# Performance work log

Measured on AMD Instinct MI355X. Metric: run time of the kernel, lower is better.

Reference implementation:

```python
import jax, jax.numpy as jnp
import numpy as np

EN_HID = 1024
DE_HID = 1024
BATCH = 64
SRC_LEN = 2048


def setup_inputs() -> dict:
    key = jax.random.key(0)
    ks = jax.random.split(key, 7)
    s_en = 1.0 / np.sqrt(EN_HID)
    s_de = 1.0 / np.sqrt(DE_HID)
    return {
        "hidden": jax.random.normal(ks[0], (1, BATCH, DE_HID), jnp.float32),
        "en_output": jax.random.normal(ks[1], (BATCH, SRC_LEN, EN_HID), jnp.float32),
        "w_en_w": jax.random.uniform(ks[2], (DE_HID, EN_HID), jnp.float32, -s_en, s_en),
        "w_en_b": jax.random.uniform(ks[3], (DE_HID,), jnp.float32, -s_en, s_en),
        "w_de_w": jax.random.uniform(ks[4], (DE_HID, DE_HID), jnp.float32, -s_de, s_de),
        "w_de_b": jax.random.uniform(ks[5], (DE_HID,), jnp.float32, -s_de, s_de),
        "v_w": jax.random.uniform(ks[6], (1, DE_HID), jnp.float32, -s_de, s_de),
    }


def reference(hidden, en_output, w_en_w, w_en_b, w_de_w, w_de_b, v_w):
    # hidden: (1, B, Dd) -> (B, 1, Dd); broadcast over src_len instead of repeat
    h = jnp.transpose(hidden, (1, 0, 2))  # (B, 1, Dd)
    proj_en = jnp.einsum('bse,de->bsd', en_output, w_en_w) + w_en_b  # (B, S, Dd)
    proj_de = jnp.einsum('bqh,dh->bqd', h, w_de_w) + w_de_b          # (B, 1, Dd)
    energy = jnp.tanh(proj_en + proj_de)                              # (B, S, Dd)
    scores = jnp.einsum('bsd,od->bs', energy, v_w)                   # (B, S)
    attention = jax.nn.softmax(scores, axis=1)                        # (B, S)
    weighted = jnp.einsum('bs,bse->be', attention, en_output)[:, None, :]  # (B, 1, E)
    return weighted, attention
```

## Files before the change

### kernel.cpp

```cpp
#include <hip/hip_runtime.h>
#include <stdint.h>

typedef __attribute__((ext_vector_type(4))) float  f32x4;
typedef __attribute__((ext_vector_type(8))) short  bf16x8;
typedef __attribute__((ext_vector_type(4))) short  s16x4;

#define BATCH   64
#define SRC_LEN 2048
#define HID     1024
#define M_TOT   (BATCH*SRC_LEN)

#define BM 256
#define BN 256
#define BK 64

__device__ __forceinline__ short f2bf(float f) {
  unsigned u = __builtin_bit_cast(unsigned, f);
  u += 0x7fffu + ((u >> 16) & 1u);
  return (short)(u >> 16);
}
__device__ __forceinline__ float bf2f(short s) {
  unsigned u = ((unsigned)(unsigned short)s) << 16;
  return __builtin_bit_cast(float, u);
}

__global__ void k_convert_w(const float* __restrict__ w, short* __restrict__ wb) {
  int i = (blockIdx.x * 256 + threadIdx.x) * 8;
  f32x4 a = *(const f32x4*)(w + i);
  f32x4 b = *(const f32x4*)(w + i + 4);
  bf16x8 o;
  o[0]=f2bf(a[0]); o[1]=f2bf(a[1]); o[2]=f2bf(a[2]); o[3]=f2bf(a[3]);
  o[4]=f2bf(b[0]); o[5]=f2bf(b[1]); o[6]=f2bf(b[2]); o[7]=f2bf(b[3]);
  *(bf16x8*)(wb + i) = o;
}

__global__ void k_convert_en(const float* __restrict__ in, short* __restrict__ out) {
  size_t stride = (size_t)gridDim.x * 256 * 8;
  size_t base = ((size_t)blockIdx.x * 256 + threadIdx.x) * 8;
  size_t total = (size_t)M_TOT * HID;
  for (; base < total; base += stride) {
    f32x4 a = *(const f32x4*)(in + base);
    f32x4 b = *(const f32x4*)(in + base + 4);
    bf16x8 o;
    o[0]=f2bf(a[0]); o[1]=f2bf(a[1]); o[2]=f2bf(a[2]); o[3]=f2bf(a[3]);
    o[4]=f2bf(b[0]); o[5]=f2bf(b[1]); o[6]=f2bf(b[2]); o[7]=f2bf(b[3]);
    *(bf16x8*)(out + base) = o;
  }
}

__global__ void k_bias(const float* __restrict__ hidden, const float* __restrict__ w_de_w,
                       const float* __restrict__ w_en_b, const float* __restrict__ w_de_b,
                       float* __restrict__ bias_all) {
  __shared__ float hid[HID];
  int b  = blockIdx.x >> 2;
  int dc = blockIdx.x & 3;
  for (int i = threadIdx.x; i < HID; i += 256) hid[i] = hidden[b*HID + i];
  __syncthreads();
  int d = dc*256 + threadIdx.x;
  const f32x4* wrow = (const f32x4*)(w_de_w + (size_t)d*HID);
  float acc = 0.f;
  #pragma unroll 8
  for (int q = 0; q < HID/4; ++q) {
    f32x4 w4 = wrow[q];
    f32x4 h4 = *(const f32x4*)&hid[q*4];
    acc += w4[0]*h4[0] + w4[1]*h4[1] + w4[2]*h4[2] + w4[3]*h4[3];
  }
  bias_all[b*HID + d] = acc + w_en_b[d] + w_de_b[d];
}

__global__ void __launch_bounds__(512, 1) k_gemm_score_fast(
    const short* __restrict__ Abf,
    const short* __restrict__ Bw,
    const float* __restrict__ bias_all,
    const float* __restrict__ v_w,
    float* __restrict__ scores)
{
  __shared__ short As[2][BM][BK];
  __shared__ short Bs[2][BN][BK];

  int raw  = blockIdx.x;
  int xcd  = raw & 7;
  int idx  = raw >> 3;
  int mblk = xcd * 64 + (idx >> 2);
  int nblk = idx & 3;
  int m0 = mblk * BM, n0 = nblk * BN;

  int tid  = threadIdx.x;
  int lane = tid & 63;
  int wid  = tid >> 6;
  int wm = wid >> 2, wn = wid & 3;
  int fr  = lane & 15;
  int fko = (lane >> 4) * 8;
  int rsw = (fr & 7) << 3;

  f32x4 acc[8][4] = {};

  int cA0 = tid,        cA1 = tid + 1024;
  int cA2 = tid + 512,  cA3 = tid + 1536;
  int gb  = ((tid >> 8) << 9) + (tid & 255);
  int cB0 = gb,         cB1 = gb + 1024;
  int cB2 = gb + 256,   cB3 = gb + 1280;

  #define SOFF(c, rb) ((size_t)((rb) + ((c) >> 3)) * HID + (size_t)((((c) & 7) ^ (((c) >> 3) & 7)) * 8))
  const size_t sA0 = SOFF(cA0, m0), sA1 = SOFF(cA1, m0), sA2 = SOFF(cA2, m0), sA3 = SOFF(cA3, m0);
  const size_t sB0 = SOFF(cB0, n0), sB1 = SOFF(cB1, n0), sB2 = SOFF(cB2, n0), sB3 = SOFF(cB3, n0);
  #undef SOFF

  #define GLD(SRCP, LDSBASE, DOFF) __builtin_amdgcn_global_load_lds( \
      (const __attribute__((address_space(1))) void*)(SRCP), \
      (__attribute__((address_space(3))) void*)((char*)(LDSBASE) + (DOFF)), 16, 0, 0)

  #define STG_A01(OTH, KT) do{ GLD(Abf + sA0 + (KT)*64, &As[OTH][0][0], cA0*16); \
                               GLD(Abf + sA1 + (KT)*64, &As[OTH][0][0], cA1*16); }while(0)
  #define STG_A23(OTH, KT) do{ GLD(Abf + sA2 + (KT)*64, &As[OTH][0][0], cA2*16); \
                               GLD(Abf + sA3 + (KT)*64, &As[OTH][0][0], cA3*16); }while(0)
  #define STG_B01(OTH, KT) do{ GLD(Bw  + sB0 + (KT)*64, &Bs[OTH][0][0], cB0*16); \
                               GLD(Bw  + sB1 + (KT)*64, &Bs[OTH][0][0], cB1*16); }while(0)
  #define STG_B23(OTH, KT) do{ GLD(Bw  + sB2 + (KT)*64, &Bs[OTH][0][0], cB2*16); \
                               GLD(Bw  + sB3 + (KT)*64, &Bs[OTH][0][0], cB3*16); }while(0)

  bf16x8 aF[8], bF[4];
  #define LDA(BUF, MQ) { _Pragma("unroll") for (int mi = 0; mi < 4; ++mi) \
      _Pragma("unroll") for (int kk = 0; kk < 2; ++kk) \
        aF[mi*2+kk] = *(const bf16x8*)&As[BUF][wm*128 + (MQ)*64 + mi*16 + fr][(kk*32 + fko) ^ rsw]; }
  #define LDB(BUF, NQ) { _Pragma("unroll") for (int ni = 0; ni < 2; ++ni) \
      _Pragma("unroll") for (int kk = 0; kk < 2; ++kk) \
        bF[ni*2+kk] = *(const bf16x8*)&Bs[BUF][wn*64 + (NQ)*32 + ni*16 + fr][(kk*32 + fko) ^ rsw]; }
  #define MMQ(MQ, NQ) { _Pragma("unroll") for (int mi = 0; mi < 4; ++mi) \
      _Pragma("unroll") for (int ni = 0; ni < 2; ++ni) \
      _Pragma("unroll") for (int kk = 0; kk < 2; ++kk) \
        acc[(MQ)*4+mi][(NQ)*2+ni] = __builtin_amdgcn_mfma_f32_16x16x32_bf16( \
            aF[mi*2+kk], bF[ni*2+kk], acc[(MQ)*4+mi][(NQ)*2+ni], 0, 0, 0); }

  #define BARR   __builtin_amdgcn_s_barrier()
  #define VMC(N) asm volatile("s_waitcnt vmcnt(" #N ")" ::: "memory")
  #define PR1    __builtin_amdgcn_s_setprio(1)
  #define PR0    __builtin_amdgcn_s_setprio(0)

  STG_A01(0, 0); STG_B01(0, 0); STG_B23(0, 0); STG_A23(0, 0);
  VMC(4); BARR;

  #pragma unroll 1
  for (int kt = 0; kt < 15; ++kt) {
    int buf = kt & 1, oth = buf ^ 1;
    LDA(buf, 0); LDB(buf, 0); STG_A01(oth, kt + 1);
    BARR; PR1; MMQ(0, 0); PR0; VMC(4); BARR;
    LDB(buf, 1); STG_B01(oth, kt + 1);
    BARR; PR1; MMQ(0, 1); PR0; VMC(4); BARR;
    LDA(buf, 1); STG_B23(oth, kt + 1);
    BARR; PR1; MMQ(1, 1); PR0; BARR;
    LDB(buf, 0); STG_A23(oth, kt + 1);
    BARR; PR1; MMQ(1, 0); PR0; VMC(4); BARR;
  }
  LDA(1, 0); LDB(1, 0); BARR; PR1; MMQ(0, 0); PR0; VMC(2); BARR;
  LDB(1, 1);            BARR; PR1; MMQ(0, 1); PR0; VMC(0); BARR;
  LDA(1, 1);            BARR; PR1; MMQ(1, 1); PR0; BARR;
  LDB(1, 0);            BARR; PR1; MMQ(1, 0); PR0;

  #undef LDA
  #undef LDB
  #undef MMQ
  #undef STG_A01
  #undef STG_A23
  #undef STG_B01
  #undef STG_B23
  #undef GLD

  int b = m0 >> 11;
  float vv[4], bb[4];
  #pragma unroll
  for (int nf = 0; nf < 4; ++nf) {
    int col = n0 + wn*64 + nf*16 + fr;
    vv[nf] = v_w[col];
    bb[nf] = bias_all[b*HID + col];
  }
  #pragma unroll
  for (int mf = 0; mf < 8; ++mf) {
    #pragma unroll
    for (int j = 0; j < 4; ++j) {
      float p = 0.f;
      #pragma unroll
      for (int nf = 0; nf < 4; ++nf)
        p += tanhf(acc[mf][nf][j] + bb[nf]) * vv[nf];
      p += __shfl_xor(p, 1);
      p += __shfl_xor(p, 2);
      p += __shfl_xor(p, 4);
      p += __shfl_xor(p, 8);
      if (fr == 0) {
        int row = wm*128 + mf*16 + ((lane >> 4) << 2) + j;
        atomicAdd(&scores[m0 + row], p);
      }
    }
  }
}

__global__ void __launch_bounds__(256) k_gemm_score_conv(
    const float* __restrict__ A, const short* __restrict__ Bw,
    const float* __restrict__ bias_all, const float* __restrict__ v_w,
    float* __restrict__ scores)
{
  __shared__ short Asl[128][64];
  __shared__ short Bsl[128][64];
  int raw  = blockIdx.x;
  int xcd  = raw & 7;
  int idx  = raw >> 3;
  int mblk = xcd * (M_TOT/128/8) + (idx >> 3);
  int nblk = idx & 7;
  int m0 = mblk * 128, n0 = nblk * 128;
  int tid  = threadIdx.x;
  int lane = tid & 63;
  int wid  = tid >> 6;
  int wr = wid >> 1, wc = wid & 1;
  int fr  = lane & 15;
  int fko = (lane >> 4) * 8;
  f32x4 acc[4][4] = {};
  int ar = tid >> 1;
  int ac = (tid & 1) * 32;
  const float* aBase = A + (size_t)(m0 + ar) * HID + ac;
  f32x4 aReg[8];
  #pragma unroll
  for (int i = 0; i < 8; ++i) aReg[i] = *(const f32x4*)(aBase + i*4);
  for (int kt = 0; kt < 16; ++kt) {
    __syncthreads();
    #pragma unroll
    for (int g = 0; g < 4; ++g) {
      bf16x8 w;
      w[0]=f2bf(aReg[2*g][0]);   w[1]=f2bf(aReg[2*g][1]);
      w[2]=f2bf(aReg[2*g][2]);   w[3]=f2bf(aReg[2*g][3]);
      w[4]=f2bf(aReg[2*g+1][0]); w[5]=f2bf(aReg[2*g+1][1]);
      w[6]=f2bf(aReg[2*g+1][2]); w[7]=f2bf(aReg[2*g+1][3]);
      *(bf16x8*)&Asl[ar][ac + g*8] = w;
    }
    #pragma unroll
    for (int j = 0; j < 4; ++j) {
      int c = j*256 + tid;
      const short* src = Bw + (size_t)(n0 + (c >> 3)) * HID + kt*64 + (c & 7)*8;
      __builtin_amdgcn_global_load_lds(
          (const __attribute__((address_space(1))) void*)src,
          (__attribute__((address_space(3))) void*)((char*)&Bsl[0][0] + c*16),
          16, 0, 0);
    }
    __syncthreads();
    if (kt + 1 < 16) {
      const float* nxt = aBase + (kt+1)*64;
      #pragma unroll
      for (int i = 0; i < 8; ++i) aReg[i] = *(const f32x4*)(nxt + i*4);
    }
    #pragma unroll
    for (int kk = 0; kk < 2; ++kk) {
      bf16x8 aF[4], bF[4];
      #pragma unroll
      for (int mi = 0; mi < 4; ++mi)
        aF[mi] = *(const bf16x8*)&Asl[wr*64 + mi*16 + fr][kk*32 + fko];
      #pragma unroll
      for (int ni = 0; ni < 4; ++ni)
        bF[ni] = *(const bf16x8*)&Bsl[wc*64 + ni*16 + fr][kk*32 + fko];
      #pragma unroll
      for (int mi = 0; mi < 4; ++mi)
        #pragma unroll
        for (int ni = 0; ni < 4; ++ni)
          acc[mi][ni] = __builtin_amdgcn_mfma_f32_16x16x32_bf16(aF[mi], bF[ni], acc[mi][ni], 0, 0, 0);
    }
  }
  int b = m0 >> 11;
  float vv[4], bb[4];
  #pragma unroll
  for (int ni = 0; ni < 4; ++ni) {
    int col = n0 + wc*64 + ni*16 + fr;
    vv[ni] = v_w[col];
    bb[ni] = bias_all[b*HID + col];
  }
  #pragma unroll
  for (int mi = 0; mi < 4; ++mi) {
    #pragma unroll
    for (int j = 0; j < 4; ++j) {
      float p = 0.f;
      #pragma unroll
      for (int ni = 0; ni < 4; ++ni)
        p += tanhf(acc[mi][ni][j] + bb[ni]) * vv[ni];
      p += __shfl_xor(p, 1);
      p += __shfl_xor(p, 2);
      p += __shfl_xor(p, 4);
      p += __shfl_xor(p, 8);
      if (fr == 0) {
        int row = wr*64 + mi*16 + ((lane >> 4) << 2) + j;
        atomicAdd(&scores[m0 + row], p);
      }
    }
  }
}

__global__ void k_softmax(float* __restrict__ attn) {
  int b = blockIdx.x;
  float* row = attn + (size_t)b * SRC_LEN;
  int tid = threadIdx.x, lane = tid & 63, wid = tid >> 6;
  __shared__ float red[4];
  float v[8];
  #pragma unroll
  for (int i = 0; i < 8; ++i) v[i] = row[tid + i*256];
  float mx = v[0];
  #pragma unroll
  for (int i = 1; i < 8; ++i) mx = fmaxf(mx, v[i]);
  #pragma unroll
  for (int o = 32; o; o >>= 1) mx = fmaxf(mx, __shfl_xor(mx, o));
  if (lane == 0) red[wid] = mx;
  __syncthreads();
  mx = fmaxf(fmaxf(red[0], red[1]), fmaxf(red[2], red[3]));
  float s = 0.f;
  #pragma unroll
  for (int i = 0; i < 8; ++i) { v[i] = __expf(v[i] - mx); s += v[i]; }
  #pragma unroll
  for (int o = 32; o; o >>= 1) s += __shfl_xor(s, o);
  __syncthreads();
  if (lane == 0) red[wid] = s;
  __syncthreads();
  s = red[0] + red[1] + red[2] + red[3];
  float inv = 1.f / s;
  #pragma unroll
  for (int i = 0; i < 8; ++i) row[tid + i*256] = v[i] * inv;
}

__global__ void k_weighted_bf(const short* __restrict__ en_bf, const float* __restrict__ attn,
                              float* __restrict__ outw) {
  int b  = blockIdx.x >> 4;
  int sc = blockIdx.x & 15;
  __shared__ float aw[128];
  int tid = threadIdx.x;
  if (tid < 128) aw[tid] = attn[b*SRC_LEN + sc*128 + tid];
  __syncthreads();
  const short* base = en_bf + ((size_t)b*SRC_LEN + sc*128) * HID + tid*4;
  float a0=0.f, a1=0.f, a2=0.f, a3=0.f;
  #pragma unroll 8
  for (int s = 0; s < 128; ++s) {
    s16x4 x = *(const s16x4*)(base + (size_t)s*HID);
    float w = aw[s];
    a0 += w*bf2f(x[0]); a1 += w*bf2f(x[1]); a2 += w*bf2f(x[2]); a3 += w*bf2f(x[3]);
  }
  float* o = outw + b*HID + tid*4;
  atomicAdd(o+0, a0); atomicAdd(o+1, a1);
  atomicAdd(o+2, a2); atomicAdd(o+3, a3);
}

__global__ void k_weighted(const float* __restrict__ en, const float* __restrict__ attn,
                           float* __restrict__ outw) {
  int b  = blockIdx.x >> 4;
  int sc = blockIdx.x & 15;
  __shared__ float aw[128];
  int tid = threadIdx.x;
  if (tid < 128) aw[tid] = attn[b*SRC_LEN + sc*128 + tid];
  __syncthreads();
  const float* base = en + ((size_t)b*SRC_LEN + sc*128) * HID + tid*4;
  f32x4 acc = {0.f, 0.f, 0.f, 0.f};
  #pragma unroll 8
  for (int s = 0; s < 128; ++s) {
    f32x4 x = *(const f32x4*)(base + (size_t)s*HID);
    float w = aw[s];
    acc[0] += w*x[0]; acc[1] += w*x[1]; acc[2] += w*x[2]; acc[3] += w*x[3];
  }
  float* o = outw + b*HID + tid*4;
  atomicAdd(o+0, acc[0]); atomicAdd(o+1, acc[1]);
  atomicAdd(o+2, acc[2]); atomicAdd(o+3, acc[3]);
}

extern "C" void kernel_launch(void* const* d_in, const int* in_sizes, int n_in,
                              void* d_out, int out_size, void* d_ws, size_t ws_size,
                              hipStream_t stream) {
  const float* hidden = (const float*)d_in[0];
  const float* en     = (const float*)d_in[1];
  const float* w_en_w = (const float*)d_in[2];
  const float* w_en_b = (const float*)d_in[3];
  const float* w_de_w = (const float*)d_in[4];
  const float* w_de_b = (const float*)d_in[5];
  const float* v_w    = (const float*)d_in[6];

  float* outw = (float*)d_out;
  float* attn = outw + BATCH*HID;

  const size_t en_elems = (size_t)M_TOT * HID;
  const size_t need_fast = en_elems*sizeof(short) + (size_t)HID*HID*sizeof(short)
                         + (size_t)BATCH*HID*sizeof(float);

  hipMemsetAsync(d_out, 0, (size_t)out_size * sizeof(float), stream);

  if (ws_size >= need_fast) {
    short* en_bf    = (short*)d_ws;
    short* w_bf     = en_bf + en_elems;
    float* bias_all = (float*)(w_bf + (size_t)HID*HID);

    k_convert_en<<<dim3(2048), dim3(256), 0, stream>>>(en, en_bf);
    k_convert_w<<<dim3(HID*HID/(256*8)), dim3(256), 0, stream>>>(w_en_w, w_bf);
    k_bias<<<dim3(BATCH*4), dim3(256), 0, stream>>>(hidden, w_de_w, w_en_b, w_de_b, bias_all);
    k_gemm_score_fast<<<dim3((M_TOT/BM)*(HID/BN)), dim3(512), 0, stream>>>(en_bf, w_bf, bias_all, v_w, attn);
    k_softmax<<<dim3(BATCH), dim3(256), 0, stream>>>(attn);
    k_weighted_bf<<<dim3(BATCH*16), dim3(256), 0, stream>>>(en_bf, attn, outw);
  } else {
    short* w_bf     = (short*)d_ws;
    float* bias_all = (float*)((char*)d_ws + (size_t)HID*HID*sizeof(short));
    k_convert_w<<<dim3(HID*HID/(256*8)), dim3(256), 0, stream>>>(w_en_w, w_bf);
    k_bias<<<dim3(BATCH*4), dim3(256), 0, stream>>>(hidden, w_de_w, w_en_b, w_de_b, bias_all);
    k_gemm_score_conv<<<dim3((M_TOT/128)*(HID/128)), dim3(256), 0, stream>>>(en, w_bf, bias_all, v_w, attn);
    k_softmax<<<dim3(BATCH), dim3(256), 0, stream>>>(attn);
    k_weighted<<<dim3(BATCH*16), dim3(256), 0, stream>>>(en, attn, outw);
  }
}
```

Measured before the change: 608.8 us.

## Fuse fp32-to-bf16 conversion of encoder outputs into the score GEMM

Removes the separate conversion kernel for en_output. The GEMM now loads fp32 A tiles into registers, converts them to bf16 and writes them into LDS, and one N-block per tile also writes the bf16 copy to global memory for the later weighted-sum kernel. The B tiles still use direct global-to-LDS loads. The main loop is rescheduled around register-staged A loads, and the aim is to save a full read and write pass over the large activation tensor. In exchange, the GEMM reads twice as many A bytes (fp32), is read by four N-blocks, and carries extra conversion ALU work and register pressure.

Result: slower. 646.5 us (+6.2%).

```diff
diff --git a/kernel.cpp b/kernel.cpp
--- a/kernel.cpp
+++ b/kernel.cpp
@@ -23,29 +23,18 @@
   unsigned u = ((unsigned)(unsigned short)s) << 16;
   return __builtin_bit_cast(float, u);
 }
+__device__ __forceinline__ bf16x8 cvt8(f32x4 lo, f32x4 hi) {
+  bf16x8 o;
+  o[0]=f2bf(lo[0]); o[1]=f2bf(lo[1]); o[2]=f2bf(lo[2]); o[3]=f2bf(lo[3]);
+  o[4]=f2bf(hi[0]); o[5]=f2bf(hi[1]); o[6]=f2bf(hi[2]); o[7]=f2bf(hi[3]);
+  return o;
+}
 
 __global__ void k_convert_w(const float* __restrict__ w, short* __restrict__ wb) {
   int i = (blockIdx.x * 256 + threadIdx.x) * 8;
   f32x4 a = *(const f32x4*)(w + i);
   f32x4 b = *(const f32x4*)(w + i + 4);
-  bf16x8 o;
-  o[0]=f2bf(a[0]); o[1]=f2bf(a[1]); o[2]=f2bf(a[2]); o[3]=f2bf(a[3]);
-  o[4]=f2bf(b[0]); o[5]=f2bf(b[1]); o[6]=f2bf(b[2]); o[7]=f2bf(b[3]);
-  *(bf16x8*)(wb + i) = o;
-}
-
-__global__ void k_convert_en(const float* __restrict__ in, short* __restrict__ out) {
-  size_t stride = (size_t)gridDim.x * 256 * 8;
-  size_t base = ((size_t)blockIdx.x * 256 + threadIdx.x) * 8;
-  size_t total = (size_t)M_TOT * HID;
-  for (; base < total; base += stride) {
-    f32x4 a = *(const f32x4*)(in + base);
-    f32x4 b = *(const f32x4*)(in + base + 4);
-    bf16x8 o;
-    o[0]=f2bf(a[0]); o[1]=f2bf(a[1]); o[2]=f2bf(a[2]); o[3]=f2bf(a[3]);
-    o[4]=f2bf(b[0]); o[5]=f2bf(b[1]); o[6]=f2bf(b[2]); o[7]=f2bf(b[3]);
-    *(bf16x8*)(out + base) = o;
-  }
+  *(bf16x8*)(wb + i) = cvt8(a, b);
 }
 
 __global__ void k_bias(const float* __restrict__ hidden, const float* __restrict__ w_de_w,
@@ -68,12 +57,13 @@
   bias_all[b*HID + d] = acc + w_en_b[d] + w_de_b[d];
 }
 
-__global__ void __launch_bounds__(512, 1) k_gemm_score_fast(
-    const short* __restrict__ Abf,
+__global__ void __launch_bounds__(512, 1) k_gemm_score_fused(
+    const float* __restrict__ Af,
     const short* __restrict__ Bw,
     const float* __restrict__ bias_all,
     const float* __restrict__ v_w,
-    float* __restrict__ scores)
+    float* __restrict__ scores,
+    short* __restrict__ en_bf)
 {
   __shared__ short As[2][BM][BK];
   __shared__ short Bs[2][BN][BK];
@@ -95,29 +85,18 @@
 
   f32x4 acc[8][4] = {};
 
-  int cA0 = tid,        cA1 = tid + 1024;
-  int cA2 = tid + 512,  cA3 = tid + 1536;
-  int gb  = ((tid >> 8) << 9) + (tid & 255);
-  int cB0 = gb,         cB1 = gb + 1024;
-  int cB2 = gb + 256,   cB3 = gb + 1280;
-
-  #define SOFF(c, rb) ((size_t)((rb) + ((c) >> 3)) * HID + (size_t)((((c) & 7) ^ (((c) >> 3) & 7)) * 8))
-  const size_t sA0 = SOFF(cA0, m0), sA1 = SOFF(cA1, m0), sA2 = SOFF(cA2, m0), sA3 = SOFF(cA3, m0);
-  const size_t sB0 = SOFF(cB0, n0), sB1 = SOFF(cB1, n0), sB2 = SOFF(cB2, n0), sB3 = SOFF(cB3, n0);
-  #undef SOFF
-
-  #define GLD(SRCP, LDSBASE, DOFF) __builtin_amdgcn_global_load_lds( \
+  int r  = tid >> 3;
+  int sl = tid & 7;
+  int xr = sl ^ (r & 7);
+  size_t offBase = (size_t)(m0 + r) * HID + (size_t)sl * 8;
+  int    wBase   = r * BK + xr * 8;
+  int gbRow = r + ((tid >> 8) << 5);
+  size_t sBase = (size_t)(n0 + gbRow) * HID + (size_t)xr * 8;
+  int gb = ((tid >> 8) << 9) + (tid & 255);
+
+  #define GLD(SRCP, LDSP) __builtin_amdgcn_global_load_lds( \
       (const __attribute__((address_space(1))) void*)(SRCP), \
-      (__attribute__((address_space(3))) void*)((char*)(LDSBASE) + (DOFF)), 16, 0, 0)
-
-  #define STG_A01(OTH, KT) do{ GLD(Abf + sA0 + (KT)*64, &As[OTH][0][0], cA0*16); \
-                               GLD(Abf + sA1 + (KT)*64, &As[OTH][0][0], cA1*16); }while(0)
-  #define STG_A23(OTH, KT) do{ GLD(Abf + sA2 + (KT)*64, &As[OTH][0][0], cA2*16); \
-                               GLD(Abf + sA3 + (KT)*64, &As[OTH][0][0], cA3*16); }while(0)
-  #define STG_B01(OTH, KT) do{ GLD(Bw  + sB0 + (KT)*64, &Bs[OTH][0][0], cB0*16); \
-                               GLD(Bw  + sB1 + (KT)*64, &Bs[OTH][0][0], cB1*16); }while(0)
-  #define STG_B23(OTH, KT) do{ GLD(Bw  + sB2 + (KT)*64, &Bs[OTH][0][0], cB2*16); \
-                               GLD(Bw  + sB3 + (KT)*64, &Bs[OTH][0][0], cB3*16); }while(0)
+      (__attribute__((address_space(3))) void*)(LDSP), 16, 0, 0)
 
   bf16x8 aF[8], bF[4];
   #define LDA(BUF, MQ) { _Pragma("unroll") for (int mi = 0; mi < 4; ++mi) \
@@ -133,37 +112,97 @@
             aF[mi*2+kk], bF[ni*2+kk], acc[(MQ)*4+mi][(NQ)*2+ni], 0, 0, 0); }
 
   #define BARR   __builtin_amdgcn_s_barrier()
+  #define LG0    asm volatile("s_waitcnt lgkmcnt(0)" ::: "memory")
   #define VMC(N) asm volatile("s_waitcnt vmcnt(" #N ")" ::: "memory")
   #define PR1    __builtin_amdgcn_s_setprio(1)
   #define PR0    __builtin_amdgcn_s_setprio(0)
 
-  STG_A01(0, 0); STG_B01(0, 0); STG_B23(0, 0); STG_A23(0, 0);
-  VMC(4); BARR;
+  {
+    short* ldsA = (short*)&As[0][0][0] + wBase;
+    char*  ldsB = (char*)&Bs[0][0][0] + gb*16;
+    f32x4 a0 = *(const f32x4*)(Af + offBase);
+    f32x4 a1 = *(const f32x4*)(Af + offBase + 4);
+    f32x4 a2 = *(const f32x4*)(Af + offBase + 128*HID);
+    f32x4 a3 = *(const f32x4*)(Af + offBase + 128*HID + 4);
+    GLD(Bw + sBase,            ldsB + 0);
+    GLD(Bw + sBase + 128*HID,  ldsB + 16384);
+    bf16x8 av0 = cvt8(a0, a1), av1 = cvt8(a2, a3);
+    *(bf16x8*)(ldsA)        = av0;
+    *(bf16x8*)(ldsA + 8192) = av1;
+    if (nblk == 0) *(bf16x8*)(en_bf + offBase) = av0;
+    if (nblk == 1) *(bf16x8*)(en_bf + offBase + 128*HID) = av1;
+    f32x4 b0 = *(const f32x4*)(Af + offBase + 64*HID);
+    f32x4 b1 = *(const f32x4*)(Af + offBase + 64*HID + 4);
+    f32x4 b2 = *(const f32x4*)(Af + offBase + 192*HID);
+    f32x4 b3 = *(const f32x4*)(Af + offBase + 192*HID + 4);
+    GLD(Bw + sBase + 32*HID,   ldsB + 4096);
+    GLD(Bw + sBase + 160*HID,  ldsB + 20480);
+    bf16x8 av2 = cvt8(b0, b1), av3 = cvt8(b2, b3);
+    *(bf16x8*)(ldsA + 4096)  = av2;
+    *(bf16x8*)(ldsA + 12288) = av3;
+    if (nblk == 2) *(bf16x8*)(en_bf + offBase + 64*HID) = av2;
+    if (nblk == 3) *(bf16x8*)(en_bf + offBase + 192*HID) = av3;
+    LG0; BARR;
+  }
 
   #pragma unroll 1
   for (int kt = 0; kt < 15; ++kt) {
-    int buf = kt & 1, oth = buf ^ 1;
-    LDA(buf, 0); LDB(buf, 0); STG_A01(oth, kt + 1);
-    BARR; PR1; MMQ(0, 0); PR0; VMC(4); BARR;
-    LDB(buf, 1); STG_B01(oth, kt + 1);
-    BARR; PR1; MMQ(0, 1); PR0; VMC(4); BARR;
-    LDA(buf, 1); STG_B23(oth, kt + 1);
-    BARR; PR1; MMQ(1, 1); PR0; BARR;
-    LDB(buf, 0); STG_A23(oth, kt + 1);
-    BARR; PR1; MMQ(1, 0); PR0; VMC(4); BARR;
-  }
-  LDA(1, 0); LDB(1, 0); BARR; PR1; MMQ(0, 0); PR0; VMC(2); BARR;
-  LDB(1, 1);            BARR; PR1; MMQ(0, 1); PR0; VMC(0); BARR;
-  LDA(1, 1);            BARR; PR1; MMQ(1, 1); PR0; BARR;
-  LDB(1, 0);            BARR; PR1; MMQ(1, 0); PR0;
+    const int buf = kt & 1, oth = buf ^ 1;
+    const int k1 = (kt + 1) * BK;
+    short* ldsA = (short*)&As[0][0][0] + oth * (BM*BK) + wBase;
+    char*  ldsB = (char*)&Bs[0][0][0] + oth * (BN*BK*2) + gb*16;
+
+    f32x4 a0 = *(const f32x4*)(Af + offBase + k1);
+    f32x4 a1 = *(const f32x4*)(Af + offBase + k1 + 4);
+    f32x4 a2 = *(const f32x4*)(Af + offBase + 128*HID + k1);
+    f32x4 a3 = *(const f32x4*)(Af + offBase + 128*HID + k1 + 4);
+    LDA(buf, 0); LDB(buf, 0);
+    PR1; MMQ(0, 0); PR0;
+    if (nblk < 2) { VMC(4); } else { VMC(5); }
+    BARR;
+
+    GLD(Bw + sBase + k1,           ldsB + 0);
+    GLD(Bw + sBase + 128*HID + k1, ldsB + 16384);
+    bf16x8 av0 = cvt8(a0, a1), av1 = cvt8(a2, a3);
+    *(bf16x8*)(ldsA)        = av0;
+    *(bf16x8*)(ldsA + 8192) = av1;
+    if (nblk == 0) *(bf16x8*)(en_bf + offBase + k1) = av0;
+    if (nblk == 1) *(bf16x8*)(en_bf + offBase + 128*HID + k1) = av1;
+    f32x4 b0 = *(const f32x4*)(Af + offBase + 64*HID + k1);
+    f32x4 b1 = *(const f32x4*)(Af + offBase + 64*HID + k1 + 4);
+    f32x4 b2 = *(const f32x4*)(Af + offBase + 192*HID + k1);
+    f32x4 b3 = *(const f32x4*)(Af + offBase + 192*HID + k1 + 4);
+    LDB(buf, 1);
+    PR1; MMQ(0, 1); PR0;
+
+    GLD(Bw + sBase + 32*HID + k1,  ldsB + 4096);
+    GLD(Bw + sBase + 160*HID + k1, ldsB + 20480);
+    LDA(buf, 1);
+    PR1; MMQ(1, 1); PR0;
+
+    LDB(buf, 0);
+    bf16x8 av2 = cvt8(b0, b1), av3 = cvt8(b2, b3);
+    *(bf16x8*)(ldsA + 4096)  = av2;
+    *(bf16x8*)(ldsA + 12288) = av3;
+    if (nblk == 2) *(bf16x8*)(en_bf + offBase + 64*HID + k1) = av2;
+    if (nblk == 3) *(bf16x8*)(en_bf + offBase + 192*HID + k1) = av3;
+    PR1; MMQ(1, 0); PR0;
+    LG0; BARR;
+  }
+
+  LDA(1, 0); LDB(1, 0);
+  PR1; MMQ(0, 0); PR0;
+  VMC(0); BARR;
+  LDB(1, 1);
+  PR1; MMQ(0, 1); PR0;
+  LDA(1, 1);
+  PR1; MMQ(1, 1); PR0;
+  LDB(1, 0);
+  PR1; MMQ(1, 0); PR0;
 
   #undef LDA
   #undef LDB
   #undef MMQ
-  #undef STG_A01
-  #undef STG_A23
-  #undef STG_B01
-  #undef STG_B23
   #undef GLD
 
   int b = m0 >> 11;
@@ -223,14 +262,8 @@
   for (int kt = 0; kt < 16; ++kt) {
     __syncthreads();
     #pragma unroll
-    for (int g = 0; g < 4; ++g) {
-      bf16x8 w;
-      w[0]=f2bf(aReg[2*g][0]);   w[1]=f2bf(aReg[2*g][1]);
-      w[2]=f2bf(aReg[2*g][2]);   w[3]=f2bf(aReg[2*g][3]);
-      w[4]=f2bf(aReg[2*g+1][0]); w[5]=f2bf(aReg[2*g+1][1]);
-      w[6]=f2bf(aReg[2*g+1][2]); w[7]=f2bf(aReg[2*g+1][3]);
-      *(bf16x8*)&Asl[ar][ac + g*8] = w;
-    }
+    for (int g = 0; g < 4; ++g)
+      *(bf16x8*)&Asl[ar][ac + g*8] = cvt8(aReg[2*g], aReg[2*g+1]);
     #pragma unroll
     for (int j = 0; j < 4; ++j) {
       int c = j*256 + tid;
@@ -387,10 +420,10 @@
     short* w_bf     = en_bf + en_elems;
     float* bias_all = (float*)(w_bf + (size_t)HID*HID);
 
-    k_convert_en<<<dim3(2048), dim3(256), 0, stream>>>(en, en_bf);
     k_convert_w<<<dim3(HID*HID/(256*8)), dim3(256), 0, stream>>>(w_en_w, w_bf);
     k_bias<<<dim3(BATCH*4), dim3(256), 0, stream>>>(hidden, w_de_w, w_en_b, w_de_b, bias_all);
-    k_gemm_score_fast<<<dim3((M_TOT/BM)*(HID/BN)), dim3(512), 0, stream>>>(en_bf, w_bf, bias_all, v_w, attn);
+    k_gemm_score_fused<<<dim3((M_TOT/BM)*(HID/BN)), dim3(512), 0, stream>>>(
+        en, w_bf, bias_all, v_w, attn, en_bf);
     k_softmax<<<dim3(BATCH), dim3(256), 0, stream>>>(attn);
     k_weighted_bf<<<dim3(BATCH*16), dim3(256), 0, stream>>>(en_bf, attn, outw);
   } else {
```
